# Optimization experiments

Hardware: AMD Instinct MI355X
Metric: run time of the kernel (lower is better)

## Reference

```python
import jax, jax.numpy as jnp
import numpy as np

B, T, D_MODEL = 2, 2048, 2048
NUM_HEADS, NUM_KV_HEADS, HEAD_DIM = 16, 16, 128
NUM_Q_HEADS = 2 * NUM_HEADS  # diff-v2 doubles the query heads


def _rope_freqs(seqlen, dim_half, base=10000.0):
    inv = 1.0 / (base ** (np.arange(0, dim_half, dtype=np.float32) / dim_half))
    t = np.arange(seqlen, dtype=np.float32)
    ang = np.outer(t, inv)  # [T, dim_half]
    return jnp.asarray(np.cos(ang)), jnp.asarray(np.sin(ang))


def apply_rotary_interleaved(x, cos, sin):
    # x: [B, T, H, D]; cos/sin: [T, D//2]; pairs are adjacent (interleaved=True)
    x1, x2 = x[..., 0::2], x[..., 1::2]
    c = cos[None, :, None, :]
    s = sin[None, :, None, :]
    o1 = x1 * c - x2 * s
    o2 = x1 * s + x2 * c
    return jnp.stack([o1, o2], axis=-1).reshape(x.shape)


def setup_inputs() -> dict:
    key = jax.random.key(0)
    ks = jax.random.split(key, 6)
    x = jax.random.normal(ks[0], (B, T, D_MODEL), dtype=jnp.float32)
    cos, sin = _rope_freqs(T, HEAD_DIM // 2)
    sc = 1.0 / np.sqrt(D_MODEL)
    Wq = jax.random.normal(ks[1], (D_MODEL, NUM_Q_HEADS * HEAD_DIM), dtype=jnp.float32) * sc
    Wk = jax.random.normal(ks[2], (D_MODEL, NUM_KV_HEADS * HEAD_DIM), dtype=jnp.float32) * sc
    Wv = jax.random.normal(ks[3], (D_MODEL, NUM_KV_HEADS * HEAD_DIM), dtype=jnp.float32) * sc
    Wo = jax.random.normal(ks[4], (NUM_HEADS * HEAD_DIM, D_MODEL), dtype=jnp.float32) * sc
    Wlam = jax.random.normal(ks[5], (D_MODEL, NUM_HEADS), dtype=jnp.float32) * sc
    return {"x": x, "cos": cos, "sin": sin, "Wq": Wq, "Wk": Wk, "Wv": Wv, "Wo": Wo, "Wlam": Wlam}


def reference(x, cos, sin, Wq, Wk, Wv, Wo, Wlam):
    b, t, _ = x.shape
    q = (x @ Wq).reshape(b, t, NUM_Q_HEADS, HEAD_DIM)
    k = (x @ Wk).reshape(b, t, NUM_KV_HEADS, HEAD_DIM)
    v = (x @ Wv).reshape(b, t, NUM_KV_HEADS, HEAD_DIM)
    q = apply_rotary_interleaved(q, cos, sin)
    k = apply_rotary_interleaved(k, cos, sin)
    # GQA: repeat kv heads to match the doubled query heads
    rep = NUM_Q_HEADS // NUM_KV_HEADS
    k = jnp.repeat(k, rep, axis=2)
    v = jnp.repeat(v, rep, axis=2)
    scale = 1.0 / np.sqrt(HEAD_DIM)
    scores = jnp.einsum('bthd,bshd->bhts', q, k) * scale  # [B, 2H, T, T]
    causal = jnp.tril(jnp.ones((t, t), dtype=bool))
    scores = jnp.where(causal[None, None], scores, jnp.finfo(scores.dtype).min)
    p = jax.nn.softmax(scores, axis=-1)
    attn = jnp.einsum('bhts,bshd->bthd', p, v)  # [B, T, 2H, D]
    lam = jax.nn.sigmoid(x @ Wlam)  # [B, T, H]
    attn1, attn2 = attn[:, :, 0::2], attn[:, :, 1::2]
    out = attn1 - lam[..., None] * attn2  # [B, T, H, D]
    return out.reshape(b, t, NUM_HEADS * HEAD_DIM) @ Wo
```

## Files before the change

### kernel.cpp

```cpp
#include <hip/hip_runtime.h>

#define T_SEQ 2048
#define BATCH 2
#define DMODEL 2048
#define NQH 32
#define NKVH 16
#define HD 128

typedef _Float16 f16;
typedef _Float16 f16x8 __attribute__((ext_vector_type(8)));
typedef _Float16 f16x4 __attribute__((ext_vector_type(4)));
typedef _Float16 f16x2 __attribute__((ext_vector_type(2)));
typedef float f32x4 __attribute__((ext_vector_type(4)));

typedef const __attribute__((address_space(1))) void* gptr_t;
typedef __attribute__((address_space(3))) void* sptr_t;
#define GLDS16(g, l) __builtin_amdgcn_global_load_lds((gptr_t)(g), (sptr_t)(l), 16, 0, 0)

__global__ __launch_bounds__(256) void k_transpose_all(const float* __restrict__ Wq,
                                                       const float* __restrict__ Wk,
                                                       const float* __restrict__ Wv,
                                                       const float* __restrict__ Wo,
                                                       f16* __restrict__ WqkvT,
                                                       f16* __restrict__ WoT) {
  __shared__ float tile[32][33];
  const int z = blockIdx.z;
  const float* W;
  f16* WT;
  int N;
  if (z == 0)      { W = Wq; WT = WqkvT;                          N = 4096; }
  else if (z == 1) { W = Wk; WT = WqkvT + (size_t)4096 * 2048;    N = 2048; }
  else if (z == 2) { W = Wv; WT = WqkvT + (size_t)6144 * 2048;    N = 2048; }
  else             { W = Wo; WT = WoT;                            N = 2048; }
  const int K = 2048;
  int n0 = blockIdx.x * 32;
  if (n0 >= N) return;
  int k0 = blockIdx.y * 32;
  int tx = threadIdx.x & 31;
  int ty0 = threadIdx.x >> 5;
  #pragma unroll
  for (int i = 0; i < 4; ++i) {
    int ty = ty0 + i * 8;
    tile[ty][tx] = W[(size_t)(k0 + ty) * N + n0 + tx];
  }
  __syncthreads();
  #pragma unroll
  for (int i = 0; i < 4; ++i) {
    int ty = ty0 + i * 8;
    WT[(size_t)(n0 + ty) * K + k0 + tx] = (f16)tile[tx][ty];
  }
}

template<int BM, int BN, int WM, int WN, int THREADS, int OM>
__global__ __launch_bounds__(THREADS, 2) void k_gemm2(const f16* __restrict__ A,
                                                      const f16* __restrict__ BT,
                                                      void* __restrict__ C0,
                                                      f16* __restrict__ Kh,
                                                      f16* __restrict__ VTg,
                                                      const float* __restrict__ cosb,
                                                      const float* __restrict__ sinb,
                                                      int M, int N, int K) {
  constexpr int MR = BM / WM / 16;
  constexpr int NR = BN / WN / 16;
  constexpr int ACH = BM * 64 / 8 / THREADS;
  constexpr int BCH = BN * 64 / 8 / THREADS;
  static_assert(ACH + BCH == 8, "vmcnt constant assumes 8 loads/thread/stage");
  __shared__ alignas(16) f16 Al[2][BM * 64];
  __shared__ alignas(16) f16 Bl[2][BN * 64];
  const int tid = threadIdx.x;
  const int lane = tid & 63;
  const int w = tid >> 6;
  const int wr = w / WN, wc = w % WN;
  const int lr = lane & 15, lg = lane >> 4;
  const int nbx = N / BN;
  const int cpx = gridDim.x >> 3;
  const int wg = (blockIdx.x & 7) * cpx + (blockIdx.x >> 3);
  const int m0 = (wg / nbx) * BM, n0 = (wg % nbx) * BN;

  auto STAGE = [&](int buf, int kk) {
    #pragma unroll
    for (int q = 0; q < ACH; ++q) {
      int idx = q * THREADS + tid;
      int r = idx >> 3, g = idx & 7;
      GLDS16(A + (size_t)(m0 + r) * K + kk + ((g ^ (r & 7)) * 8), &Al[buf][idx * 8]);
    }
    #pragma unroll
    for (int q = 0; q < BCH; ++q) {
      int idx = q * THREADS + tid;
      int r = idx >> 3, g = idx & 7;
      GLDS16(BT + (size_t)(n0 + r) * K + kk + ((g ^ (r & 7)) * 8), &Bl[buf][idx * 8]);
    }
  };

  f32x4 acc[MR][NR] = {};
  STAGE(0, 0);
  const int nt = K / 64;
  #pragma unroll 2
  for (int t = 0; t < nt; ++t) {
    const int buf = t & 1;
    if (t + 1 < nt) {
      STAGE(buf ^ 1, (t + 1) * 64);
      __builtin_amdgcn_sched_barrier(0);
      asm volatile("s_waitcnt vmcnt(8)" ::: "memory");
    } else {
      __builtin_amdgcn_sched_barrier(0);
      asm volatile("s_waitcnt vmcnt(0)" ::: "memory");
    }
    __builtin_amdgcn_s_barrier();
    __builtin_amdgcn_sched_barrier(0);
    #pragma unroll
    for (int kh = 0; kh < 2; ++kh) {
      f16x8 af[MR], bf[NR];
      #pragma unroll
      for (int i = 0; i < MR; ++i) {
        int r = wr * (BM / WM) + i * 16 + lr;
        af[i] = *(const f16x8*)&Al[buf][r * 64 + (((kh * 4 + lg) ^ (r & 7)) * 8)];
      }
      #pragma unroll
      for (int j = 0; j < NR; ++j) {
        int r = wc * (BN / WN) + j * 16 + lr;
        bf[j] = *(const f16x8*)&Bl[buf][r * 64 + (((kh * 4 + lg) ^ (r & 7)) * 8)];
      }
      #pragma unroll
      for (int i = 0; i < MR; ++i)
        #pragma unroll
        for (int j = 0; j < NR; ++j)
          acc[i][j] = __builtin_amdgcn_mfma_f32_16x16x32_f16(af[i], bf[j], acc[i][j], 0, 0, 0);
    }
    __builtin_amdgcn_sched_barrier(0);
    __builtin_amdgcn_s_barrier();
    __builtin_amdgcn_sched_barrier(0);
  }

  const int mb = m0 + wr * (BM / WM);
  const int nb = n0 + wc * (BN / WN);
  if constexpr (OM == 0) {
    float* C = (float*)C0;
    #pragma unroll
    for (int i = 0; i < MR; ++i)
      #pragma unroll
      for (int j = 0; j < NR; ++j) {
        int r0 = mb + i * 16 + lg * 4;
        int c = nb + j * 16 + lr;
        #pragma unroll
        for (int r = 0; r < 4; ++r)
          C[(size_t)(r0 + r) * N + c] = acc[i][j][r];
      }
  } else {
    if (n0 < 6144) {
      f16* dst = (n0 < 4096) ? (f16*)C0 : Kh;
      const int ncols = (n0 < 4096) ? 4096 : 2048;
      const int coff = (n0 < 4096) ? 0 : 4096;
      #pragma unroll
      for (int i = 0; i < MR; ++i)
        #pragma unroll
        for (int j = 0; j < NR; ++j) {
          int c = nb + j * 16 + lr - coff;
          int jp = (c & 127) >> 1;
          bool odd = (c & 1);
          #pragma unroll
          for (int r = 0; r < 4; ++r) {
            int row = mb + i * 16 + lg * 4 + r;
            int t = row & (T_SEQ - 1);
            float v = acc[i][j][r];
            float pv = __shfl_xor(v, 1);
            float cs = cosb[t * 64 + jp], sn = sinb[t * 64 + jp];
            float out = odd ? (pv * sn + v * cs) : (v * cs - pv * sn);
            dst[(size_t)row * ncols + c] = (f16)out;
          }
        }
    } else {
      #pragma unroll
      for (int i = 0; i < MR; ++i)
        #pragma unroll
        for (int j = 0; j < NR; ++j) {
          int c = nb + j * 16 + lr - 6144;
          int head = c >> 7, d = c & 127;
          int row0 = mb + i * 16 + lg * 4;
          int bb = row0 >> 11, t0 = row0 & (T_SEQ - 1);
          f16x4 zv;
          #pragma unroll
          for (int r = 0; r < 4; ++r) zv[r] = (f16)acc[i][j][r];
          *(f16x4*)(VTg + ((size_t)(bb * NKVH + head) * HD + d) * T_SEQ + t0) = zv;
        }
    }
  }
}

__global__ __launch_bounds__(256) void k_lambda_conv(const float* __restrict__ x,
                                                     const float* __restrict__ Wlam,
                                                     float* __restrict__ lam,
                                                     f16* __restrict__ xh) {
  int row = blockIdx.x;
  const float* xr = x + (size_t)row * DMODEL;
  const int e = threadIdx.x * 8;
  const float4* xp = (const float4*)(xr + e);
  float4 a = xp[0], b2 = xp[1];
  float xv[8] = {a.x, a.y, a.z, a.w, b2.x, b2.y, b2.z, b2.w};
  f16x8 hv;
  #pragma unroll
  for (int j = 0; j < 8; ++j) hv[j] = (f16)xv[j];
  *(f16x8*)(xh + (size_t)row * DMODEL + e) = hv;
  float acc[16];
  #pragma unroll
  for (int h = 0; h < 16; ++h) acc[h] = 0.f;
  #pragma unroll
  for (int j = 0; j < 8; ++j) {
    const float4* wp = (const float4*)(Wlam + (size_t)(e + j) * 16);
    #pragma unroll
    for (int g = 0; g < 4; ++g) {
      float4 wv = wp[g];
      acc[g * 4 + 0] += xv[j] * wv.x; acc[g * 4 + 1] += xv[j] * wv.y;
      acc[g * 4 + 2] += xv[j] * wv.z; acc[g * 4 + 3] += xv[j] * wv.w;
    }
  }
  #pragma unroll
  for (int h = 0; h < 16; ++h)
    for (int off = 32; off > 0; off >>= 1)
      acc[h] += __shfl_down(acc[h], off);
  __shared__ float part[4][16];
  int lane = threadIdx.x & 63, w = threadIdx.x >> 6;
  if (lane == 0) {
    #pragma unroll
    for (int h = 0; h < 16; ++h) part[w][h] = acc[h];
  }
  __syncthreads();
  if (threadIdx.x < 16) {
    float s = part[0][threadIdx.x] + part[1][threadIdx.x] + part[2][threadIdx.x] + part[3][threadIdx.x];
    lam[row * 16 + threadIdx.x] = 1.f / (1.f + __expf(-s));
  }
}

__global__ __launch_bounds__(512, 4) void k_attn6(const f16* __restrict__ Q,
                                                  const f16* __restrict__ K,
                                                  const f16* __restrict__ VT,
                                                  const float* __restrict__ lam,
                                                  f16* __restrict__ Z) {
  __shared__ f16 Kl[64 * 128];
  __shared__ f16 Vl[128 * 64];
  __shared__ f16 Pl[8][16][40];
  __shared__ f16 Po[4][16][136];
  const int tid = threadIdx.x;
  const int lane = tid & 63;
  const int w = tid >> 6;
  const int lr = lane & 15, lg = lane >> 4;
  const int flat = blockIdx.x;
  const int xcd = flat & 7;
  const int work = xcd * 64 + (flat >> 3);
  const int grp = work >> 4;
  const int bx = work & 15;
  const int b = grp >> 4, hkv = grp & 15;
  const int h = hkv * 2 + (w >> 2);
  const int wq = w & 3;
  const int kvstride = NKVH * HD;
  const f16* Kg  = K  + (size_t)b * T_SEQ * kvstride + hkv * HD;
  const f16* VTg = VT + (size_t)(b * NKVH + hkv) * HD * T_SEQ;
  const float sc = 0.08838834764831845f;

  #pragma unroll 1
  for (int half = 0; half < 2; ++half) {
    const int qt = half ? (31 - bx) : bx;
    const int qb = qt * 64;
    const int qw = qb + wq * 16;
    const int qrow = qw + lr;
    f16x8 qf[4];
    {
      const f16* qp = Q + (size_t)(b * T_SEQ + qrow) * (NQH * HD) + h * HD + lg * 8;
      #pragma unroll
      for (int c = 0; c < 4; ++c) qf[c] = *(const f16x8*)(qp + c * 32);
    }
    f32x4 o[8] = {};
    float mi = -1e30f, li = 0.f;

    const int nt = qt + 1;
    #pragma unroll
    for (int q = 0; q < 2; ++q) {
      int idx = q * 512 + tid;
      int r = idx >> 4, g = idx & 15;
      GLDS16(Kg + (size_t)r * kvstride + (g ^ (r & 7)) * 8, &Kl[idx * 8]);
    }
    #pragma unroll
    for (int q = 0; q < 2; ++q) {
      int idx = q * 512 + tid;
      int d = idx >> 3, g = idx & 7;
      GLDS16(VTg + (size_t)d * T_SEQ + (g ^ (d & 7)) * 8, &Vl[idx * 8]);
    }
    __syncthreads();

    #pragma unroll 1
    for (int t = 0; t < nt; ++t) {
      const int s0 = t * 64;
      const bool pf = (t + 1 < nt);
      f16x8 ka[2], va[2];
      if (pf) {
        const int s1 = s0 + 64;
        #pragma unroll
        for (int q = 0; q < 2; ++q) {
          int idx = q * 512 + tid;
          int r = idx >> 4, g = idx & 15;
          ka[q] = *(const f16x8*)(Kg + (size_t)(s1 + r) * kvstride + g * 8);
        }
        #pragma unroll
        for (int q = 0; q < 2; ++q) {
          int idx = q * 512 + tid;
          int d = idx >> 3, g = idx & 7;
          va[q] = *(const f16x8*)(VTg + (size_t)d * T_SEQ + s1 + g * 8);
        }
      }
      f32x4 sf[4] = {};
      __builtin_amdgcn_s_setprio(1);
      #pragma unroll
      for (int c = 0; c < 4; ++c) {
        #pragma unroll
        for (int nb = 0; nb < 4; ++nb) {
          f16x8 kf = *(const f16x8*)&Kl[(((nb * 16 + lr) * 16) + ((c * 4 + lg) ^ (lr & 7))) * 8];
          sf[nb] = __builtin_amdgcn_mfma_f32_16x16x32_f16(kf, qf[c], sf[nb], 0, 0, 0);
        }
      }
      __builtin_amdgcn_s_setprio(0);
      float v[16];
      #pragma unroll
      for (int nb = 0; nb < 4; ++nb)
        #pragma unroll
        for (int rr = 0; rr < 4; ++rr) {
          float x = sf[nb][rr] * sc;
          int kv = s0 + nb * 16 + lg * 4 + rr;
          v[nb * 4 + rr] = (kv > qrow) ? -1e30f : x;
        }
      float pm = v[0];
      #pragma unroll
      for (int i = 1; i < 16; ++i) pm = fmaxf(pm, v[i]);
      pm = fmaxf(pm, __shfl_xor(pm, 16));
      pm = fmaxf(pm, __shfl_xor(pm, 32));
      const bool nogrow = (__all(pm <= mi + 8.0f) != 0);
      const float mnew = nogrow ? mi : fmaxf(mi, pm);
      float rs = 0.f;
      #pragma unroll
      for (int i = 0; i < 16; ++i) { float p = __expf(v[i] - mnew); v[i] = p; rs += p; }
      rs += __shfl_xor(rs, 16);
      rs += __shfl_xor(rs, 32);
      if (nogrow) {
        li += rs;
      } else {
        float a = __expf(mi - mnew);
        mi = mnew;
        li = a * li + rs;
        float ab[4];
        #pragma unroll
        for (int rr = 0; rr < 4; ++rr) ab[rr] = __shfl(a, lg * 4 + rr);
        #pragma unroll
        for (int j = 0; j < 8; ++j)
          #pragma unroll
          for (int rr = 0; rr < 4; ++rr) o[j][rr] *= ab[rr];
      }
      #pragma unroll
      for (int ks = 0; ks < 2; ++ks) {
        #pragma unroll
        for (int nb2 = 0; nb2 < 2; ++nb2) {
          int nb = ks * 2 + nb2;
          f16x4 pk;
          #pragma unroll
          for (int rr = 0; rr < 4; ++rr) pk[rr] = (f16)v[nb * 4 + rr];
          *(f16x4*)&Pl[w][lr][nb2 * 16 + lg * 4] = pk;
        }
        f16x8 pa = *(const f16x8*)&Pl[w][lr][lg * 8];
        __builtin_amdgcn_s_setprio(1);
        #pragma unroll
        for (int j = 0; j < 8; ++j) {
          f16x8 vbj = *(const f16x8*)&Vl[(((j * 16 + lr) * 8) + ((ks * 4 + lg) ^ (lr & 7))) * 8];
          o[j] = __builtin_amdgcn_mfma_f32_16x16x32_f16(pa, vbj, o[j], 0, 0, 0);
        }
        __builtin_amdgcn_s_setprio(0);
      }
      __syncthreads();
      if (pf) {
        #pragma unroll
        for (int q = 0; q < 2; ++q) {
          int idx = q * 512 + tid;
          int r = idx >> 4, g = idx & 15;
          *(f16x8*)&Kl[(r * 16 + (g ^ (r & 7))) * 8] = ka[q];
        }
        #pragma unroll
        for (int q = 0; q < 2; ++q) {
          int idx = q * 512 + tid;
          int d = idx >> 3, g = idx & 7;
          *(f16x8*)&Vl[(d * 8 + (g ^ (d & 7))) * 8] = va[q];
        }
      }
      __syncthreads();
    }
    float lib[4];
    #pragma unroll
    for (int rr = 0; rr < 4; ++rr) lib[rr] = 1.f / __shfl(li, lg * 4 + rr);
    if (w >= 4) {
      #pragma unroll
      for (int j = 0; j < 8; ++j)
        #pragma unroll
        for (int rr = 0; rr < 4; ++rr)
          Po[wq][lg * 4 + rr][j * 16 + lr] = (f16)(o[j][rr] * lib[rr]);
    }
    __syncthreads();
    if (w < 4) {
      float lamv[4];
      #pragma unroll
      for (int rr = 0; rr < 4; ++rr)
        lamv[rr] = lam[(size_t)(b * T_SEQ + qw + lg * 4 + rr) * 16 + hkv];
      #pragma unroll
      for (int j = 0; j < 8; ++j)
        #pragma unroll
        for (int rr = 0; rr < 4; ++rr) {
          float a1 = o[j][rr] * lib[rr];
          float a2 = (float)Po[wq][lg * 4 + rr][j * 16 + lr];
          Z[(size_t)(b * T_SEQ + qw + lg * 4 + rr) * 2048 + hkv * 128 + j * 16 + lr] =
              (f16)(a1 - lamv[rr] * a2);
        }
    }
    __syncthreads();
  }
}

extern "C" void kernel_launch(void* const* d_in, const int* in_sizes, int n_in,
                              void* d_out, int out_size, void* d_ws, size_t ws_size,
                              hipStream_t stream) {
  const float* x    = (const float*)d_in[0];
  const float* cosb = (const float*)d_in[1];
  const float* sinb = (const float*)d_in[2];
  const float* Wq   = (const float*)d_in[3];
  const float* Wk   = (const float*)d_in[4];
  const float* Wv   = (const float*)d_in[5];
  const float* Wo   = (const float*)d_in[6];
  const float* Wlam = (const float*)d_in[7];

  char* ws = (char*)d_ws;
  f16*  xh     = (f16*)(ws);
  f16*  WqkvT  = (f16*)(ws + 16777216);
  f16*  WoT    = (f16*)(ws + 50331648);
  f16*  Qh     = (f16*)(ws + 58720256);
  f16*  Kh     = (f16*)(ws + 92274688);
  f16*  VTg    = (f16*)(ws + 109051904);
  f16*  Zh     = (f16*)(ws + 159383552);
  float* lam   = (float*)(ws + 176160768);

  k_transpose_all<<<dim3(128, 64, 4), 256, 0, stream>>>(Wq, Wk, Wv, Wo, WqkvT, WoT);
  k_lambda_conv<<<4096, 256, 0, stream>>>(x, Wlam, lam, xh);

  k_gemm2<128, 128, 2, 2, 256, 3><<<2048, 256, 0, stream>>>(xh, WqkvT, Qh, Kh, VTg,
                                                            cosb, sinb, 4096, 8192, 2048);

  k_attn6<<<512, 512, 0, stream>>>(Qh, Kh, VTg, lam, Zh);

  k_gemm2<128, 128, 2, 2, 256, 0><<<512, 256, 0, stream>>>(Zh, WoT, d_out, nullptr, nullptr,
                                                           nullptr, nullptr, 4096, 2048, 2048);
}
```

Measured before the change: 446.1 us.

## Use 256x256 8-wave ping-pong GEMM for fused QKV projection

Adds a dedicated QKV projection kernel with 256x256 tiles, 512 threads and one block per CU. It splits each K-step into four quadrant phases that interleave LDS reads, asynchronous global-to-LDS loads and MFMA bursts, with explicit waitcnt and barriers and raised priority around the MFMA bursts. The larger tile raises arithmetic intensity and the phased schedule aims to hide load latency behind MFMA work. In exchange, occupancy drops, register pressure rises from the 8x4 accumulator array, and the hand-written vmcnt accounting is fragile. The old templated GEMM is reduced to the plain fp32 output path used for the output projection.

Result: faster. 422.8 us (-5.2%).

```diff
diff --git a/kernel.cpp b/kernel.cpp
--- a/kernel.cpp
+++ b/kernel.cpp
@@ -51,14 +51,165 @@
   }
 }
 
-template<int BM, int BN, int WM, int WN, int THREADS, int OM>
+__global__ __launch_bounds__(512, 1) void k_gemm8p(const f16* __restrict__ A,
+                                                   const f16* __restrict__ BT,
+                                                   f16* __restrict__ Qh,
+                                                   f16* __restrict__ Kh,
+                                                   f16* __restrict__ VTg,
+                                                   const float* __restrict__ cosb,
+                                                   const float* __restrict__ sinb) {
+  const int K = 2048, N = 8192;
+  __shared__ alignas(16) f16 Al[2][256 * 64];
+  __shared__ alignas(16) f16 Bl[2][256 * 64];
+  const int tid = threadIdx.x;
+  const int lane = tid & 63;
+  const int w = tid >> 6;
+  const int wr = w >> 2, wc = w & 3;
+  const int lr = lane & 15, lg = lane >> 4;
+  const int nbx = 32;
+  const int cpx = gridDim.x >> 3;
+  const int wg = (blockIdx.x & 7) * cpx + (blockIdx.x >> 3);
+  const int m0 = (wg / nbx) * 256, n0 = (wg % nbx) * 256;
+
+#define ST_A(MH, BB, KK)                                                        \
+  { _Pragma("unroll")                                                           \
+    for (int i2 = 0; i2 < 2; ++i2) {                                            \
+      int li = i2 * 512 + tid; int rh = li >> 3, g = li & 7;                    \
+      int r = ((rh >> 6) << 7) + (MH) * 64 + (rh & 63);                         \
+      GLDS16(A + (size_t)(m0 + r) * K + (KK) + ((g ^ (r & 7)) * 8),             \
+             &Al[BB][(r * 8 + g) * 8]);                                         \
+    } }
+#define ST_B(NH, BB, KK)                                                        \
+  { _Pragma("unroll")                                                           \
+    for (int i2 = 0; i2 < 2; ++i2) {                                            \
+      int li = i2 * 512 + tid; int rh = li >> 3, g = li & 7;                    \
+      int r = ((rh >> 5) << 6) + (NH) * 32 + (rh & 31);                         \
+      GLDS16(BT + (size_t)(n0 + r) * K + (KK) + ((g ^ (r & 7)) * 8),            \
+             &Bl[BB][(r * 8 + g) * 8]);                                         \
+    } }
+#define LDA_Q(MH, BUF)                                                          \
+  { _Pragma("unroll")                                                           \
+    for (int kh = 0; kh < 2; ++kh)                                              \
+      _Pragma("unroll")                                                         \
+      for (int i = 0; i < 4; ++i) {                                             \
+        int r = wr * 128 + ((MH) * 4 + i) * 16 + lr;                            \
+        af[kh][i] = *(const f16x8*)&Al[BUF][r * 64 + (((kh * 4 + lg) ^ (r & 7)) * 8)]; \
+      } }
+#define LDB_Q(NH, BUF)                                                          \
+  { _Pragma("unroll")                                                           \
+    for (int kh = 0; kh < 2; ++kh)                                              \
+      _Pragma("unroll")                                                         \
+      for (int j = 0; j < 2; ++j) {                                             \
+        int r = wc * 64 + ((NH) * 2 + j) * 16 + lr;                             \
+        bf[kh][j] = *(const f16x8*)&Bl[BUF][r * 64 + (((kh * 4 + lg) ^ (r & 7)) * 8)]; \
+      } }
+#define FMA_Q(MH, NH)                                                           \
+  { __builtin_amdgcn_s_setprio(1);                                              \
+    _Pragma("unroll")                                                           \
+    for (int kh = 0; kh < 2; ++kh)                                              \
+      _Pragma("unroll")                                                         \
+      for (int i = 0; i < 4; ++i)                                               \
+        _Pragma("unroll")                                                       \
+        for (int j = 0; j < 2; ++j)                                             \
+          acc[(MH) * 4 + i][(NH) * 2 + j] = __builtin_amdgcn_mfma_f32_16x16x32_f16( \
+              af[kh][i], bf[kh][j], acc[(MH) * 4 + i][(NH) * 2 + j], 0, 0, 0);  \
+    __builtin_amdgcn_s_setprio(0); }
+#define BAR() __builtin_amdgcn_s_barrier()
+#define SB() __builtin_amdgcn_sched_barrier(0)
+#define LGKM0() { asm volatile("s_waitcnt lgkmcnt(0)" ::: "memory"); SB(); }
+
+  f32x4 acc[8][4] = {};
+  ST_A(0, 0, 0); ST_B(0, 0, 0); ST_B(1, 0, 0); ST_A(1, 0, 0);
+  asm volatile("s_waitcnt vmcnt(4)" ::: "memory");
+  BAR();
+
+  const int nt = K / 64;
+  #pragma unroll 2
+  for (int t = 0; t < nt; ++t) {
+    const int buf = t & 1;
+    const int kk1 = (t + 1) * 64;
+    const bool nxt = (t + 1 < nt);
+    f16x8 af[2][4], bf[2][2];
+    LDA_Q(0, buf); LDB_Q(0, buf);
+    if (nxt) ST_A(0, buf ^ 1, kk1);
+    BAR(); LGKM0();
+    FMA_Q(0, 0);
+    if (nxt) { asm volatile("s_waitcnt vmcnt(4)" ::: "memory"); }
+    else     { asm volatile("s_waitcnt vmcnt(2)" ::: "memory"); }
+    SB(); BAR(); SB();
+    LDB_Q(1, buf);
+    if (nxt) ST_B(0, buf ^ 1, kk1);
+    BAR(); LGKM0();
+    FMA_Q(0, 1);
+    if (nxt) { asm volatile("s_waitcnt vmcnt(4)" ::: "memory"); }
+    else     { asm volatile("s_waitcnt vmcnt(0)" ::: "memory"); }
+    SB(); BAR(); SB();
+    LDA_Q(1, buf); LDB_Q(0, buf);
+    if (nxt) ST_B(1, buf ^ 1, kk1);
+    BAR(); LGKM0();
+    FMA_Q(1, 0);
+    SB(); BAR(); SB();
+    LDB_Q(1, buf);
+    if (nxt) ST_A(1, buf ^ 1, kk1);
+    BAR(); LGKM0();
+    FMA_Q(1, 1);
+    if (nxt) { asm volatile("s_waitcnt vmcnt(4)" ::: "memory"); }
+    SB(); BAR(); SB();
+  }
+#undef ST_A
+#undef ST_B
+#undef LDA_Q
+#undef LDB_Q
+#undef FMA_Q
+#undef BAR
+#undef SB
+#undef LGKM0
+
+  const int mb = m0 + wr * 128;
+  const int nb = n0 + wc * 64;
+  if (n0 < 6144) {
+    f16* dst = (n0 < 4096) ? Qh : Kh;
+    const int ncols = (n0 < 4096) ? 4096 : 2048;
+    const int coff = (n0 < 4096) ? 0 : 4096;
+    #pragma unroll
+    for (int i = 0; i < 8; ++i)
+      #pragma unroll
+      for (int j = 0; j < 4; ++j) {
+        int c = nb + j * 16 + lr - coff;
+        int jp = (c & 127) >> 1;
+        bool odd = (c & 1);
+        #pragma unroll
+        for (int r = 0; r < 4; ++r) {
+          int row = mb + i * 16 + lg * 4 + r;
+          int t = row & (T_SEQ - 1);
+          float v = acc[i][j][r];
+          float pv = __shfl_xor(v, 1);
+          float cs = cosb[t * 64 + jp], sn = sinb[t * 64 + jp];
+          float out = odd ? (pv * sn + v * cs) : (v * cs - pv * sn);
+          dst[(size_t)row * ncols + c] = (f16)out;
+        }
+      }
+  } else {
+    #pragma unroll
+    for (int i = 0; i < 8; ++i)
+      #pragma unroll
+      for (int j = 0; j < 4; ++j) {
+        int c = nb + j * 16 + lr - 6144;
+        int head = c >> 7, d = c & 127;
+        int row0 = mb + i * 16 + lg * 4;
+        int bb = row0 >> 11, t0 = row0 & (T_SEQ - 1);
+        f16x4 zv;
+        #pragma unroll
+        for (int r = 0; r < 4; ++r) zv[r] = (f16)acc[i][j][r];
+        *(f16x4*)(VTg + ((size_t)(bb * NKVH + head) * HD + d) * T_SEQ + t0) = zv;
+      }
+  }
+}
+
+template<int BM, int BN, int WM, int WN, int THREADS>
 __global__ __launch_bounds__(THREADS, 2) void k_gemm2(const f16* __restrict__ A,
                                                       const f16* __restrict__ BT,
-                                                      void* __restrict__ C0,
-                                                      f16* __restrict__ Kh,
-                                                      f16* __restrict__ VTg,
-                                                      const float* __restrict__ cosb,
-                                                      const float* __restrict__ sinb,
+                                                      float* __restrict__ C,
                                                       int M, int N, int K) {
   constexpr int MR = BM / WM / 16;
   constexpr int NR = BN / WN / 16;
@@ -134,57 +285,16 @@
 
   const int mb = m0 + wr * (BM / WM);
   const int nb = n0 + wc * (BN / WN);
-  if constexpr (OM == 0) {
-    float* C = (float*)C0;
-    #pragma unroll
-    for (int i = 0; i < MR; ++i)
-      #pragma unroll
-      for (int j = 0; j < NR; ++j) {
-        int r0 = mb + i * 16 + lg * 4;
-        int c = nb + j * 16 + lr;
-        #pragma unroll
-        for (int r = 0; r < 4; ++r)
-          C[(size_t)(r0 + r) * N + c] = acc[i][j][r];
-      }
-  } else {
-    if (n0 < 6144) {
-      f16* dst = (n0 < 4096) ? (f16*)C0 : Kh;
-      const int ncols = (n0 < 4096) ? 4096 : 2048;
-      const int coff = (n0 < 4096) ? 0 : 4096;
-      #pragma unroll
-      for (int i = 0; i < MR; ++i)
-        #pragma unroll
-        for (int j = 0; j < NR; ++j) {
-          int c = nb + j * 16 + lr - coff;
-          int jp = (c & 127) >> 1;
-          bool odd = (c & 1);
-          #pragma unroll
-          for (int r = 0; r < 4; ++r) {
-            int row = mb + i * 16 + lg * 4 + r;
-            int t = row & (T_SEQ - 1);
-            float v = acc[i][j][r];
-            float pv = __shfl_xor(v, 1);
-            float cs = cosb[t * 64 + jp], sn = sinb[t * 64 + jp];
-            float out = odd ? (pv * sn + v * cs) : (v * cs - pv * sn);
-            dst[(size_t)row * ncols + c] = (f16)out;
-          }
-        }
-    } else {
-      #pragma unroll
-      for (int i = 0; i < MR; ++i)
-        #pragma unroll
-        for (int j = 0; j < NR; ++j) {
-          int c = nb + j * 16 + lr - 6144;
-          int head = c >> 7, d = c & 127;
-          int row0 = mb + i * 16 + lg * 4;
-          int bb = row0 >> 11, t0 = row0 & (T_SEQ - 1);
-          f16x4 zv;
-          #pragma unroll
-          for (int r = 0; r < 4; ++r) zv[r] = (f16)acc[i][j][r];
-          *(f16x4*)(VTg + ((size_t)(bb * NKVH + head) * HD + d) * T_SEQ + t0) = zv;
-        }
-    }
-  }
+  #pragma unroll
+  for (int i = 0; i < MR; ++i)
+    #pragma unroll
+    for (int j = 0; j < NR; ++j) {
+      int r0 = mb + i * 16 + lg * 4;
+      int c = nb + j * 16 + lr;
+      #pragma unroll
+      for (int r = 0; r < 4; ++r)
+        C[(size_t)(r0 + r) * N + c] = acc[i][j][r];
+    }
 }
 
 __global__ __launch_bounds__(256) void k_lambda_conv(const float* __restrict__ x,
@@ -444,11 +554,10 @@
   k_transpose_all<<<dim3(128, 64, 4), 256, 0, stream>>>(Wq, Wk, Wv, Wo, WqkvT, WoT);
   k_lambda_conv<<<4096, 256, 0, stream>>>(x, Wlam, lam, xh);
 
-  k_gemm2<128, 128, 2, 2, 256, 3><<<2048, 256, 0, stream>>>(xh, WqkvT, Qh, Kh, VTg,
-                                                            cosb, sinb, 4096, 8192, 2048);
+  k_gemm8p<<<512, 512, 0, stream>>>(xh, WqkvT, Qh, Kh, VTg, cosb, sinb);
 
   k_attn6<<<512, 512, 0, stream>>>(Qh, Kh, VTg, lam, Zh);
 
-  k_gemm2<128, 128, 2, 2, 256, 0><<<512, 256, 0, stream>>>(Zh, WoT, d_out, nullptr, nullptr,
-                                                           nullptr, nullptr, 4096, 2048, 2048);
+  k_gemm2<128, 128, 2, 2, 256><<<512, 256, 0, stream>>>(Zh, WoT, (float*)d_out,
+                                                        4096, 2048, 2048);
 }
```
